# Kernel optimization log

Measured on AMD Instinct MI355X. Metric: run time of the kernel, lower is better.

The kernel has to match this reference:

```python
import jax, jax.numpy as jnp
import numpy as np
import math

B, S, HID = 1, 2048, 1024
H = 16
D = HID // H          # head_dim = 64
M = 128               # RFF num_features
SIGMA = 1.0
ALPHA = 0.9
NORMALIZE = True


def setup_inputs() -> dict:
    key = jax.random.key(0)
    ks = jax.random.split(key, 12)
    s = 1.0 / math.sqrt(HID)  # nn.Linear default-ish init scale
    inp = {
        "hidden_states": jax.random.normal(ks[0], (B, S, HID), dtype=jnp.float32),
        "attention_mask": jnp.zeros((B, 1, 1, S), dtype=jnp.float32),  # 0 = attend
        "Wq": jax.random.uniform(ks[1], (HID, HID), minval=-s, maxval=s, dtype=jnp.float32),
        "bq": jnp.zeros((HID,), dtype=jnp.float32),
        "Wk": jax.random.uniform(ks[2], (HID, HID), minval=-s, maxval=s, dtype=jnp.float32),
        "bk": jnp.zeros((HID,), dtype=jnp.float32),
        "Wv": jax.random.uniform(ks[3], (HID, HID), minval=-s, maxval=s, dtype=jnp.float32),
        "bv": jnp.zeros((HID,), dtype=jnp.float32),
        "Wo": jax.random.uniform(ks[4], (HID, HID), minval=-s, maxval=s, dtype=jnp.float32),
        "bo": jnp.zeros((HID,), dtype=jnp.float32),
        # RFF kernel params per head: omega ~ N(0, 1/sigma^2), phase b ~ U[0, 2pi]
        "omega": jax.random.normal(ks[5], (H, D, M), dtype=jnp.float32) / SIGMA,
        "rff_b": jax.random.uniform(ks[6], (H, M), minval=0.0, maxval=2.0 * math.pi, dtype=jnp.float32),
    }
    return inp


def _heads(x):
    # (B, S, HID) -> (B, H, S, D)
    return x.reshape(B, S, H, D).transpose(0, 2, 1, 3)


def _phi(x, omega, rff_b):
    # x: (B, H, S, D) -> (B, H, S, M) random Fourier features
    proj = jnp.einsum("bhsd,hdm->bhsm", x, omega) + rff_b[None, :, None, :]
    phi = math.sqrt(2.0 / M) * jnp.cos(proj)
    if NORMALIZE:
        phi = phi / (jnp.linalg.norm(phi, axis=-1, keepdims=True) + 1e-6)
    return phi


def reference(hidden_states, attention_mask, Wq, bq, Wk, bk, Wv, bv, Wo, bo, omega, rff_b):
    q = _heads(hidden_states @ Wq.T + bq)   # (B,H,S,D)
    k = _heads(hidden_states @ Wk.T + bk)
    v = _heads(hidden_states @ Wv.T + bv)

    qn = q / (jnp.linalg.norm(q, axis=-1, keepdims=True) + 1e-6)
    kn = k / (jnp.linalg.norm(k, axis=-1, keepdims=True) + 1e-6)

    dot_scores = jnp.einsum("bhqd,bhkd->bhqk", q, k)             # standard QK^T
    kernel_scores = jnp.einsum("bhqm,bhkm->bhqk",
                               _phi(qn, omega, rff_b),
                               _phi(kn, omega, rff_b))            # phi(Q)phi(K)^T

    scores = (ALPHA * dot_scores + (1.0 - ALPHA) * kernel_scores) / math.sqrt(D)
    scores = scores + attention_mask * -10000.0
    weights = jax.nn.softmax(scores, axis=-1)                     # dropout: eval mode (identity)

    context = jnp.einsum("bhqk,bhkd->bhqd", weights, v)
    context = context.transpose(0, 2, 1, 3).reshape(B, S, HID)
    return context @ Wo.T + bo
```

## Files before the change

kernel.cpp:

```cpp
#include <hip/hip_runtime.h>
#include <math.h>

#define S_LEN 2048
#define HID   1024
#define NH    16
#define HD    64
#define NM    128
#define CAUG  192
#define NCH   32

constexpr float ALPHA = 0.9f;

typedef __attribute__((ext_vector_type(8))) short bf16x8;
typedef __attribute__((ext_vector_type(4))) short bf16x4;
typedef __attribute__((ext_vector_type(4))) float f32x4;
typedef __attribute__((ext_vector_type(4))) int   int4v;

#define MFMA(a,b,c) __builtin_amdgcn_mfma_f32_16x16x32_bf16(a,b,c,0,0,0)

static __device__ inline short f2bf(float f) {
    unsigned u = __float_as_uint(f);
    u += 0x7fffu + ((u >> 16) & 1u);
    return (short)(u >> 16);
}
static __device__ inline float bf2f(short s) {
    return __uint_as_float(((unsigned)(unsigned short)s) << 16);
}

__global__ __launch_bounds__(256)
void conv_kernel(const float* __restrict__ hs,
                 const float* __restrict__ Wq, const float* __restrict__ Wk,
                 const float* __restrict__ Wv, const float* __restrict__ Wo,
                 const float* __restrict__ omega,
                 short* __restrict__ hsb, short* __restrict__ wqb, short* __restrict__ wkb,
                 short* __restrict__ wvb, short* __restrict__ wob, short* __restrict__ omtb)
{
    int i = blockIdx.x * 256 + threadIdx.x;
    if (i >= 1605632) return;
    if (i >= 1572864) {
        int j = (i - 1572864) * 4;
        int h = j >> 13, rem = j & 8191;
        int d = rem >> 7, m = rem & 127;
        float4 v = *(const float4*)(omega + j);
        short* dst = omtb + ((h * 128 + m) << 6) + d;
        dst[0]       = f2bf(v.x);
        dst[64]      = f2bf(v.y);
        dst[128]     = f2bf(v.z);
        dst[192]     = f2bf(v.w);
        return;
    }
    const float* src; short* dst; int off;
    if (i < 524288) { src = hs; dst = hsb; off = i; }
    else {
        int j = i - 524288;
        int r = j >> 18;
        off = j & 262143;
        src = (r == 0) ? Wq : (r == 1) ? Wk : (r == 2) ? Wv : Wo;
        dst = (r == 0) ? wqb : (r == 1) ? wkb : (r == 2) ? wvb : wob;
    }
    float4 v = ((const float4*)src)[off];
    bf16x4 o; o[0] = f2bf(v.x); o[1] = f2bf(v.y); o[2] = f2bf(v.z); o[3] = f2bf(v.w);
    ((bf16x4*)dst)[off] = o;
}

__global__ __launch_bounds__(256)
void gemm_mfma(const short* __restrict__ A,
               const short* __restrict__ W0, const float* __restrict__ b0, void* C0,
               const short* __restrict__ W1, const float* __restrict__ b1, void* C1,
               const short* __restrict__ W2, const float* __restrict__ b2, void* C2,
               int m0_, int m1_, int m2_, int Mrows)
{
    const short* W; const float* bias; void* C; int mode;
    if (blockIdx.z == 0)      { W = W0; bias = b0; C = C0; mode = m0_; }
    else if (blockIdx.z == 1) { W = W1; bias = b1; C = C1; mode = m1_; }
    else                      { W = W2; bias = b2; C = C2; mode = m2_; }

    __shared__ short As[128][40];
    __shared__ short Bs[128][40];

    const int tid = threadIdx.x;
    const int wave = tid >> 6, lane = tid & 63;
    const int l15 = lane & 15, l4 = lane >> 4;
    const int wm = wave >> 1, wn = wave & 1;
    const int m0 = blockIdx.y * 128, n0 = blockIdx.x * 128;

    const int srow = (tid >> 2);
    const int scol = (tid & 3) * 16;

    f32x4 acc[4][4];
#pragma unroll
    for (int i = 0; i < 4; ++i)
#pragma unroll
        for (int j = 0; j < 4; ++j) acc[i][j] = (f32x4){0.f,0.f,0.f,0.f};

    int4v apre[2], bpre[2];
#pragma unroll
    for (int it = 0; it < 2; ++it) {
        apre[it] = *(const int4v*)((const char*)A + (size_t)(m0 + srow + it*64) * 2048 + scol);
        bpre[it] = *(const int4v*)((const char*)W + (size_t)(n0 + srow + it*64) * 2048 + scol);
    }

    for (int ks = 0; ks < 32; ++ks) {
        __syncthreads();
#pragma unroll
        for (int it = 0; it < 2; ++it) {
            *(int4v*)((char*)&As[0][0] + (srow + it*64) * 80 + scol) = apre[it];
            *(int4v*)((char*)&Bs[0][0] + (srow + it*64) * 80 + scol) = bpre[it];
        }
        __syncthreads();
        if (ks + 1 < 32) {
            const int kb = (ks + 1) * 64;
#pragma unroll
            for (int it = 0; it < 2; ++it) {
                apre[it] = *(const int4v*)((const char*)A + (size_t)(m0 + srow + it*64) * 2048 + kb + scol);
                bpre[it] = *(const int4v*)((const char*)W + (size_t)(n0 + srow + it*64) * 2048 + kb + scol);
            }
        }
        bf16x8 af[4], bf[4];
#pragma unroll
        for (int mi = 0; mi < 4; ++mi)
            af[mi] = *(const bf16x8*)((const char*)&As[0][0] + (wm*64 + mi*16 + l15) * 80 + l4*16);
#pragma unroll
        for (int nj = 0; nj < 4; ++nj)
            bf[nj] = *(const bf16x8*)((const char*)&Bs[0][0] + (wn*64 + nj*16 + l15) * 80 + l4*16);
#pragma unroll
        for (int mi = 0; mi < 4; ++mi)
#pragma unroll
            for (int nj = 0; nj < 4; ++nj)
                acc[mi][nj] = MFMA(af[mi], bf[nj], acc[mi][nj]);
    }

#pragma unroll
    for (int nj = 0; nj < 4; ++nj) {
        const int nglob = n0 + wn*64 + nj*16 + l15;
        const float bn = bias[nglob];
#pragma unroll
        for (int mi = 0; mi < 4; ++mi) {
            const int mbase = m0 + wm*64 + mi*16 + l4*4;
            if (mode == 0) {
#pragma unroll
                for (int r = 0; r < 4; ++r)
                    ((short*)C)[(size_t)(mbase + r) * 1024 + nglob] = f2bf(acc[mi][nj][r] + bn);
            } else if (mode == 1) {
                bf16x4 pk;
#pragma unroll
                for (int r = 0; r < 4; ++r) pk[r] = f2bf(acc[mi][nj][r] + bn);
                *(bf16x4*)((short*)C + (size_t)nglob * Mrows + mbase) = pk;
            } else {
#pragma unroll
                for (int r = 0; r < 4; ++r)
                    ((float*)C)[(size_t)(mbase + r) * 1024 + nglob] = acc[mi][nj][r] + bn;
            }
        }
    }
}

__global__ __launch_bounds__(256)
void phi2_kernel(const short* __restrict__ qbuf, const short* __restrict__ kbuf,
                 const short* __restrict__ omtb, const float* __restrict__ rffb,
                 short* __restrict__ Qa, short* __restrict__ Ka)
{
    __shared__ short om[128][72];
    __shared__ float bsh[128];

    const int src = blockIdx.z, h = blockIdx.y;
    const int s0 = blockIdx.x * 64;
    const short* X = src ? kbuf : qbuf;
    short* Out     = src ? Ka : Qa;
    const float fq   = src ? 1.0f : (ALPHA * 0.125f);
    const float fphi = src ? 1.0f : ((1.0f - ALPHA) * 0.125f);

    const int tid = threadIdx.x, wave = tid >> 6, lane = tid & 63;
    const int l15 = lane & 15, l4 = lane >> 4;

    {
        const char* gsrc = (const char*)(omtb + ((size_t)h << 13));
#pragma unroll
        for (int it = 0; it < 4; ++it) {
            int f = tid * 16 + it * 4096;
            int row = f >> 7, colb = f & 127;
            *(int4v*)((char*)&om[0][0] + row * 144 + colb) = *(const int4v*)(gsrc + f);
        }
        if (tid < 128) bsh[tid] = rffb[h * 128 + tid];
    }
    __syncthreads();

    const int srow = s0 + wave * 16 + l15;

    bf16x8 xf[2];
#pragma unroll
    for (int cs = 0; cs < 2; ++cs)
        xf[cs] = *(const bf16x8*)(X + (size_t)srow * HID + h * HD + cs * 32 + l4 * 8);

    float ss = 0.f;
#pragma unroll
    for (int cs = 0; cs < 2; ++cs)
#pragma unroll
        for (int j = 0; j < 8; ++j) { float v = bf2f(xf[cs][j]); ss = fmaf(v, v, ss); }
    ss += __shfl_xor(ss, 16);
    ss += __shfl_xor(ss, 32);
    const float inv = 1.0f / (sqrtf(ss) + 1e-6f);

    bf16x8 qn[2];
#pragma unroll
    for (int cs = 0; cs < 2; ++cs) {
        bf16x8 o, w;
#pragma unroll
        for (int j = 0; j < 8; ++j) {
            float v = bf2f(xf[cs][j]);
            o[j] = f2bf(v * inv);
            w[j] = f2bf(v * fq);
        }
        qn[cs] = o;
        *(bf16x8*)(Out + ((size_t)h * S_LEN + srow) * CAUG + cs * 32 + l4 * 8) = w;
    }

    f32x4 pacc[8];
#pragma unroll
    for (int t = 0; t < 8; ++t) pacc[t] = (f32x4){0.f,0.f,0.f,0.f};
#pragma unroll
    for (int t = 0; t < 8; ++t)
#pragma unroll
        for (int cs = 0; cs < 2; ++cs) {
            bf16x8 bf = *(const bf16x8*)((const char*)&om[0][0] + (t*16 + l15) * 144 + cs*64 + l4*16);
            pacc[t] = MFMA(qn[cs], bf, pacc[t]);
        }

    float ph[8][4];
    float ps[4] = {0.f, 0.f, 0.f, 0.f};
#pragma unroll
    for (int t = 0; t < 8; ++t) {
        const float bv = bsh[t * 16 + l15];
#pragma unroll
        for (int r = 0; r < 4; ++r) {
            float p = pacc[t][r] + bv;
            float c = 0.125f * __cosf(p);
            ph[t][r] = c;
            ps[r] = fmaf(c, c, ps[r]);
        }
    }
#pragma unroll
    for (int r = 0; r < 4; ++r) {
        ps[r] += __shfl_xor(ps[r], 1);
        ps[r] += __shfl_xor(ps[r], 2);
        ps[r] += __shfl_xor(ps[r], 4);
        ps[r] += __shfl_xor(ps[r], 8);
    }
    float inv2[4];
#pragma unroll
    for (int r = 0; r < 4; ++r) inv2[r] = fphi / (sqrtf(ps[r]) + 1e-6f);

#pragma unroll
    for (int t = 0; t < 8; ++t)
#pragma unroll
        for (int r = 0; r < 4; ++r)
            Out[((size_t)h * S_LEN + s0 + wave * 16 + l4 * 4 + r) * CAUG + 64 + t * 16 + l15]
                = f2bf(ph[t][r] * inv2[r]);
}

__global__ __launch_bounds__(256, 2)
void flash_mfma(const short* __restrict__ Qa, const short* __restrict__ Ka,
                const short* __restrict__ vt, const float* __restrict__ mask,
                short* __restrict__ ctxb)
{
    __shared__ char smem[61440];

    const int tid = threadIdx.x;
    const int wave = tid >> 6, lane = tid & 63;
    const int l15 = lane & 15, l4 = lane >> 4;
    const int g = wave >> 1, sub = wave & 1;
    const int h = blockIdx.y;
    const int q0 = blockIdx.x * 64 + sub * 32;

    char* PlW  = smem + wave * 2560;
    char* bufA = smem + 10240 + g * 25600;
    char* bufB = bufA + 12800;

    bf16x8 qf[2][6];
#pragma unroll
    for (int qj = 0; qj < 2; ++qj)
#pragma unroll
        for (int cs = 0; cs < 6; ++cs)
            qf[qj][cs] = *(const bf16x8*)(Qa + ((size_t)h * 2048 + q0 + qj*16 + l15) * CAUG + cs*32 + l4*8);

    f32x4 oacc[4][2];
#pragma unroll
    for (int di = 0; di < 4; ++di)
#pragma unroll
        for (int qj = 0; qj < 2; ++qj) oacc[di][qj] = (f32x4){0.f,0.f,0.f,0.f};
    float lsum[2] = {0.f, 0.f};

    const int t = tid & 127;
    int kr[6], kcb[6];
#pragma unroll
    for (int it = 0; it < 6; ++it) { int f = t*16 + it*2048; kr[it] = f/384; kcb[it] = f%384; }

    const char* Kg = (const char*)(Ka + (size_t)h * 2048 * CAUG);
    const char* Vg = (const char*)(vt + (size_t)h * 64 * 2048);
    const int base = g * NCH;

    int4v kpre[6];
    bf16x8 vA[4], vB[4];

    auto loadKpre = [&](int kt) {
        const char* kb = Kg + (size_t)kt * 12288;
#pragma unroll
        for (int it = 0; it < 6; ++it)
            kpre[it] = *(const int4v*)(kb + (size_t)kr[it]*384 + kcb[it]);
    };
    auto writeStage = [&](char* buf) {
#pragma unroll
        for (int it = 0; it < 6; ++it)
            *(int4v*)(buf + kr[it]*400 + kcb[it]) = kpre[it];
    };
    auto loadV = [&](bf16x8 (&dst)[4], int kt) {
#pragma unroll
        for (int di = 0; di < 4; ++di)
            dst[di] = *(const bf16x8*)(Vg + (size_t)(di*16 + l15)*4096 + kt*64 + l4*16);
    };
    auto computeChunk = [&](const char* buf, const bf16x8 (&vf)[4], int kt) {
        f32x4 sacc[2][2];
#pragma unroll
        for (int fi = 0; fi < 2; ++fi)
#pragma unroll
            for (int qj = 0; qj < 2; ++qj) sacc[fi][qj] = (f32x4){0.f,0.f,0.f,0.f};
#pragma unroll
        for (int cs = 0; cs < 6; ++cs) {
            bf16x8 ka[2];
#pragma unroll
            for (int fi = 0; fi < 2; ++fi)
                ka[fi] = *(const bf16x8*)(buf + (fi*16 + l15)*400 + cs*64 + l4*16);
#pragma unroll
            for (int fi = 0; fi < 2; ++fi)
#pragma unroll
                for (int qj = 0; qj < 2; ++qj)
                    sacc[fi][qj] = MFMA(ka[fi], qf[qj][cs], sacc[fi][qj]);
        }
#pragma unroll
        for (int fi = 0; fi < 2; ++fi) {
            float4 mk = *(const float4*)&mask[kt*32 + fi*16 + l4*4];
            float mv[4] = {mk.x * -10000.f, mk.y * -10000.f, mk.z * -10000.f, mk.w * -10000.f};
#pragma unroll
            for (int qj = 0; qj < 2; ++qj) {
                bf16x4 pk;
#pragma unroll
                for (int r = 0; r < 4; ++r) {
                    float p = __expf(sacc[fi][qj][r] + mv[r]);
                    lsum[qj] += p;
                    pk[r] = f2bf(p);
                }
                *(bf16x4*)(PlW + (qj*16 + l15)*80 + fi*32 + l4*8) = pk;
            }
        }
        bf16x8 pb[2];
#pragma unroll
        for (int qj = 0; qj < 2; ++qj)
            pb[qj] = *(const bf16x8*)(PlW + (qj*16 + l15)*80 + l4*16);
#pragma unroll
        for (int di = 0; di < 4; ++di)
#pragma unroll
            for (int qj = 0; qj < 2; ++qj)
                oacc[di][qj] = MFMA(vf[di], pb[qj], oacc[di][qj]);
    };

    loadKpre(base);
    writeStage(bufA);
    loadV(vA, base);
    __syncthreads();

    for (int i = 0; i < NCH; i += 2) {
        loadKpre(base + i + 1);
        loadV(vB, base + i + 1);
        computeChunk(bufA, vA, base + i);
        writeStage(bufB);
        __syncthreads();
        if (i + 2 < NCH) {
            loadKpre(base + i + 2);
            loadV(vA, base + i + 2);
        }
        computeChunk(bufB, vB, base + i + 1);
        if (i + 2 < NCH) writeStage(bufA);
        __syncthreads();
    }

#pragma unroll
    for (int qj = 0; qj < 2; ++qj) {
        lsum[qj] += __shfl_xor(lsum[qj], 16);
        lsum[qj] += __shfl_xor(lsum[qj], 32);
    }

    float* scrO = (float*)(smem + 10240);
    float* scrL = (float*)(smem + 36352);
    if (g == 1) {
#pragma unroll
        for (int qj = 0; qj < 2; ++qj) {
#pragma unroll
            for (int di = 0; di < 4; ++di)
                *(f32x4*)&scrO[(size_t)(sub*32 + qj*16 + l15)*68 + di*16 + l4*4] = oacc[di][qj];
            if (l4 == 0) scrL[sub*32 + qj*16 + l15] = lsum[qj];
        }
    }
    __syncthreads();
    if (g == 0) {
#pragma unroll
        for (int qj = 0; qj < 2; ++qj) {
            const float l = lsum[qj] + scrL[sub*32 + qj*16 + l15];
            const float inv = 1.0f / l;
            const int s = q0 + qj*16 + l15;
#pragma unroll
            for (int di = 0; di < 4; ++di) {
                f32x4 o2 = *(const f32x4*)&scrO[(size_t)(sub*32 + qj*16 + l15)*68 + di*16 + l4*4];
                bf16x4 ob;
#pragma unroll
                for (int r = 0; r < 4; ++r) ob[r] = f2bf((oacc[di][qj][r] + o2[r]) * inv);
                *(bf16x4*)(ctxb + (size_t)s * HID + h*64 + di*16 + l4*4) = ob;
            }
        }
    }
}

extern "C" void kernel_launch(void* const* d_in, const int* in_sizes, int n_in,
                              void* d_out, int out_size, void* d_ws, size_t ws_size,
                              hipStream_t stream)
{
    const float* hs    = (const float*)d_in[0];
    const float* mask  = (const float*)d_in[1];
    const float* Wq    = (const float*)d_in[2];
    const float* bq    = (const float*)d_in[3];
    const float* Wk    = (const float*)d_in[4];
    const float* bk    = (const float*)d_in[5];
    const float* Wv    = (const float*)d_in[6];
    const float* bv    = (const float*)d_in[7];
    const float* Wo    = (const float*)d_in[8];
    const float* bo    = (const float*)d_in[9];
    const float* omega = (const float*)d_in[10];
    const float* rffb  = (const float*)d_in[11];
    float* out = (float*)d_out;

    short* wsS = (short*)d_ws;
    short* hsb = wsS;
    short* wqb = hsb + 2097152;
    short* wkb = wqb + 1048576;
    short* wvb = wkb + 1048576;
    short* wob = wvb + 1048576;
    short* qb  = wob + 1048576;
    short* kb  = qb  + 2097152;
    short* vtb = kb  + 2097152;
    short* ctxb= vtb + 2097152;
    short* QaB = ctxb+ 2097152;
    short* KaB = QaB + 6291456;
    short* omtb= KaB + 6291456;

    conv_kernel<<<6272, 256, 0, stream>>>(hs, Wq, Wk, Wv, Wo, omega,
                                          hsb, wqb, wkb, wvb, wob, omtb);
    gemm_mfma<<<dim3(8, 16, 3), 256, 0, stream>>>(hsb, wqb, bq, qb, wkb, bk, kb, wvb, bv, vtb,
                                                  0, 0, 1, S_LEN);
    phi2_kernel<<<dim3(32, 16, 2), 256, 0, stream>>>(qb, kb, omtb, rffb, QaB, KaB);
    flash_mfma<<<dim3(32, 16), 256, 0, stream>>>(QaB, KaB, vtb, mask, ctxb);
    gemm_mfma<<<dim3(8, 16, 1), 256, 0, stream>>>(ctxb, wob, bo, out, wob, bo, out, wob, bo, out,
                                                  2, 2, 2, S_LEN);
}
```

Measured before the change: 135.8 us.

## Fuse fp32-to-bf16 conversion into GEMM loads and split flash attention over keys

The standalone conversion kernel is removed. GEMMs now read fp32 inputs and weights directly and convert them to bf16 while loading, and the GEMM tile shrinks to 64x128 so each launch has twice as many blocks. Flash attention is split into two key halves along grid z, with smaller shared memory so that four blocks can run per CU. Each half writes bf16 partial outputs and row sums, and a new merge kernel combines them. The aim is to skip the extra conversion pass and raise occupancy, at the cost of the double-buffered K/V prefetch, one extra kernel launch, and rounding the partial outputs to bf16 before the merge.

```diff
diff --git a/kernel.cpp b/kernel.cpp
--- a/kernel.cpp
+++ b/kernel.cpp
@@ -7,7 +7,7 @@
 #define HD    64
 #define NM    128
 #define CAUG  192
-#define NCH   32
+#define NCHW  16
 
 constexpr float ALPHA = 0.9f;
 
@@ -28,103 +28,85 @@
 }
 
 __global__ __launch_bounds__(256)
-void conv_kernel(const float* __restrict__ hs,
-                 const float* __restrict__ Wq, const float* __restrict__ Wk,
-                 const float* __restrict__ Wv, const float* __restrict__ Wo,
-                 const float* __restrict__ omega,
-                 short* __restrict__ hsb, short* __restrict__ wqb, short* __restrict__ wkb,
-                 short* __restrict__ wvb, short* __restrict__ wob, short* __restrict__ omtb)
+void omt_kernel(const float* __restrict__ omega, short* __restrict__ omtb)
 {
     int i = blockIdx.x * 256 + threadIdx.x;
-    if (i >= 1605632) return;
-    if (i >= 1572864) {
-        int j = (i - 1572864) * 4;
-        int h = j >> 13, rem = j & 8191;
-        int d = rem >> 7, m = rem & 127;
-        float4 v = *(const float4*)(omega + j);
-        short* dst = omtb + ((h * 128 + m) << 6) + d;
-        dst[0]       = f2bf(v.x);
-        dst[64]      = f2bf(v.y);
-        dst[128]     = f2bf(v.z);
-        dst[192]     = f2bf(v.w);
-        return;
-    }
-    const float* src; short* dst; int off;
-    if (i < 524288) { src = hs; dst = hsb; off = i; }
-    else {
-        int j = i - 524288;
-        int r = j >> 18;
-        off = j & 262143;
-        src = (r == 0) ? Wq : (r == 1) ? Wk : (r == 2) ? Wv : Wo;
-        dst = (r == 0) ? wqb : (r == 1) ? wkb : (r == 2) ? wvb : wob;
-    }
-    float4 v = ((const float4*)src)[off];
-    bf16x4 o; o[0] = f2bf(v.x); o[1] = f2bf(v.y); o[2] = f2bf(v.z); o[3] = f2bf(v.w);
-    ((bf16x4*)dst)[off] = o;
+    if (i >= 131072) return;
+    int h = i >> 13, rem = i & 8191;
+    int d = rem >> 7, m = rem & 127;
+    omtb[((h * 128 + m) << 6) + d] = f2bf(omega[i]);
 }
 
 __global__ __launch_bounds__(256)
-void gemm_mfma(const short* __restrict__ A,
-               const short* __restrict__ W0, const float* __restrict__ b0, void* C0,
-               const short* __restrict__ W1, const float* __restrict__ b1, void* C1,
-               const short* __restrict__ W2, const float* __restrict__ b2, void* C2,
+void gemm_mfma(const void* __restrict__ Ax, int a_f32,
+               const float* __restrict__ W0, const float* __restrict__ b0, void* C0,
+               const float* __restrict__ W1, const float* __restrict__ b1, void* C1,
+               const float* __restrict__ W2, const float* __restrict__ b2, void* C2,
                int m0_, int m1_, int m2_, int Mrows)
 {
-    const short* W; const float* bias; void* C; int mode;
+    const float* W; const float* bias; void* C; int mode;
     if (blockIdx.z == 0)      { W = W0; bias = b0; C = C0; mode = m0_; }
     else if (blockIdx.z == 1) { W = W1; bias = b1; C = C1; mode = m1_; }
     else                      { W = W2; bias = b2; C = C2; mode = m2_; }
 
-    __shared__ short As[128][40];
+    __shared__ short As[64][40];
     __shared__ short Bs[128][40];
 
     const int tid = threadIdx.x;
     const int wave = tid >> 6, lane = tid & 63;
     const int l15 = lane & 15, l4 = lane >> 4;
     const int wm = wave >> 1, wn = wave & 1;
-    const int m0 = blockIdx.y * 128, n0 = blockIdx.x * 128;
-
-    const int srow = (tid >> 2);
-    const int scol = (tid & 3) * 16;
-
-    f32x4 acc[4][4];
-#pragma unroll
-    for (int i = 0; i < 4; ++i)
+    const int m0 = blockIdx.y * 64, n0 = blockIdx.x * 128;
+
+    const int srow = tid >> 2;
+    const int se   = (tid & 3) * 8;
+
+    f32x4 acc[2][4];
+#pragma unroll
+    for (int i = 0; i < 2; ++i)
 #pragma unroll
         for (int j = 0; j < 4; ++j) acc[i][j] = (f32x4){0.f,0.f,0.f,0.f};
 
-    int4v apre[2], bpre[2];
-#pragma unroll
-    for (int it = 0; it < 2; ++it) {
-        apre[it] = *(const int4v*)((const char*)A + (size_t)(m0 + srow + it*64) * 2048 + scol);
-        bpre[it] = *(const int4v*)((const char*)W + (size_t)(n0 + srow + it*64) * 2048 + scol);
-    }
+    auto cvt8 = [](float4 f0, float4 f1) -> int4v {
+        bf16x8 c;
+        c[0]=f2bf(f0.x); c[1]=f2bf(f0.y); c[2]=f2bf(f0.z); c[3]=f2bf(f0.w);
+        c[4]=f2bf(f1.x); c[5]=f2bf(f1.y); c[6]=f2bf(f1.z); c[7]=f2bf(f1.w);
+        return *(int4v*)&c;
+    };
+    auto ldA = [&](int ks) -> int4v {
+        if (a_f32) {
+            const float* p = (const float*)Ax + (size_t)(m0 + srow) * 1024 + ks * 32 + se;
+            return cvt8(*(const float4*)p, *(const float4*)(p + 4));
+        }
+        return *(const int4v*)((const char*)Ax + (size_t)(m0 + srow) * 2048 + ks * 64 + se * 2);
+    };
+    auto ldW = [&](int ks, int rofs) -> int4v {
+        const float* p = W + (size_t)(n0 + rofs + srow) * 1024 + ks * 32 + se;
+        return cvt8(*(const float4*)p, *(const float4*)(p + 4));
+    };
+
+    int4v apre = ldA(0), bpre0 = ldW(0, 0), bpre1 = ldW(0, 64);
 
     for (int ks = 0; ks < 32; ++ks) {
         __syncthreads();
-#pragma unroll
-        for (int it = 0; it < 2; ++it) {
-            *(int4v*)((char*)&As[0][0] + (srow + it*64) * 80 + scol) = apre[it];
-            *(int4v*)((char*)&Bs[0][0] + (srow + it*64) * 80 + scol) = bpre[it];
-        }
+        *(int4v*)((char*)&As[0][0] + srow * 80 + se * 2) = apre;
+        *(int4v*)((char*)&Bs[0][0] + srow * 80 + se * 2) = bpre0;
+        *(int4v*)((char*)&Bs[0][0] + (64 + srow) * 80 + se * 2) = bpre1;
         __syncthreads();
         if (ks + 1 < 32) {
-            const int kb = (ks + 1) * 64;
-#pragma unroll
-            for (int it = 0; it < 2; ++it) {
-                apre[it] = *(const int4v*)((const char*)A + (size_t)(m0 + srow + it*64) * 2048 + kb + scol);
-                bpre[it] = *(const int4v*)((const char*)W + (size_t)(n0 + srow + it*64) * 2048 + kb + scol);
-            }
-        }
-        bf16x8 af[4], bf[4];
-#pragma unroll
-        for (int mi = 0; mi < 4; ++mi)
-            af[mi] = *(const bf16x8*)((const char*)&As[0][0] + (wm*64 + mi*16 + l15) * 80 + l4*16);
+            apre  = ldA(ks + 1);
+            bpre0 = ldW(ks + 1, 0);
+            bpre1 = ldW(ks + 1, 64);
+        }
+        bf16x8 af[2], bf[4];
+#pragma unroll
+        for (int mi = 0; mi < 2; ++mi)
+            af[mi] = *(const bf16x8*)((const char*)&As[0][0] + (wm*32 + mi*16 + l15) * 80 + l4*16);
 #pragma unroll
         for (int nj = 0; nj < 4; ++nj)
             bf[nj] = *(const bf16x8*)((const char*)&Bs[0][0] + (wn*64 + nj*16 + l15) * 80 + l4*16);
 #pragma unroll
-        for (int mi = 0; mi < 4; ++mi)
+        for (int mi = 0; mi < 2; ++mi)
 #pragma unroll
             for (int nj = 0; nj < 4; ++nj)
                 acc[mi][nj] = MFMA(af[mi], bf[nj], acc[mi][nj]);
@@ -135,8 +117,8 @@
         const int nglob = n0 + wn*64 + nj*16 + l15;
         const float bn = bias[nglob];
 #pragma unroll
-        for (int mi = 0; mi < 4; ++mi) {
-            const int mbase = m0 + wm*64 + mi*16 + l4*4;
+        for (int mi = 0; mi < 2; ++mi) {
+            const int mbase = m0 + wm*32 + mi*16 + l4*4;
             if (mode == 0) {
 #pragma unroll
                 for (int r = 0; r < 4; ++r)
@@ -258,23 +240,23 @@
                 = f2bf(ph[t][r] * inv2[r]);
 }
 
-__global__ __launch_bounds__(256, 2)
+__global__ __launch_bounds__(256, 4)
 void flash_mfma(const short* __restrict__ Qa, const short* __restrict__ Ka,
                 const short* __restrict__ vt, const float* __restrict__ mask,
-                short* __restrict__ ctxb)
-{
-    __shared__ char smem[61440];
+                short* __restrict__ Opart, float* __restrict__ Lpart)
+{
+    __shared__ char smem[35840];
 
     const int tid = threadIdx.x;
     const int wave = tid >> 6, lane = tid & 63;
     const int l15 = lane & 15, l4 = lane >> 4;
     const int g = wave >> 1, sub = wave & 1;
     const int h = blockIdx.y;
+    const int ksp = blockIdx.z;
     const int q0 = blockIdx.x * 64 + sub * 32;
 
-    char* PlW  = smem + wave * 2560;
-    char* bufA = smem + 10240 + g * 25600;
-    char* bufB = bufA + 12800;
+    char* Kbuf = smem + g * 12800;
+    char* PlW  = smem + 25600 + wave * 2560;
 
     bf16x8 qf[2][6];
 #pragma unroll
@@ -297,28 +279,27 @@
 
     const char* Kg = (const char*)(Ka + (size_t)h * 2048 * CAUG);
     const char* Vg = (const char*)(vt + (size_t)h * 64 * 2048);
-    const int base = g * NCH;
+    const int base = ksp * 32 + g * NCHW;
 
     int4v kpre[6];
-    bf16x8 vA[4], vB[4];
-
     auto loadKpre = [&](int kt) {
         const char* kb = Kg + (size_t)kt * 12288;
 #pragma unroll
         for (int it = 0; it < 6; ++it)
             kpre[it] = *(const int4v*)(kb + (size_t)kr[it]*384 + kcb[it]);
     };
-    auto writeStage = [&](char* buf) {
+
+    loadKpre(base);
+
+    for (int i = 0; i < NCHW; ++i) {
+        const int kt = base + i;
+        __syncthreads();
 #pragma unroll
         for (int it = 0; it < 6; ++it)
-            *(int4v*)(buf + kr[it]*400 + kcb[it]) = kpre[it];
-    };
-    auto loadV = [&](bf16x8 (&dst)[4], int kt) {
-#pragma unroll
-        for (int di = 0; di < 4; ++di)
-            dst[di] = *(const bf16x8*)(Vg + (size_t)(di*16 + l15)*4096 + kt*64 + l4*16);
-    };
-    auto computeChunk = [&](const char* buf, const bf16x8 (&vf)[4], int kt) {
+            *(int4v*)(Kbuf + kr[it]*400 + kcb[it]) = kpre[it];
+        __syncthreads();
+        if (i + 1 < NCHW) loadKpre(kt + 1);
+
         f32x4 sacc[2][2];
 #pragma unroll
         for (int fi = 0; fi < 2; ++fi)
@@ -329,7 +310,7 @@
             bf16x8 ka[2];
 #pragma unroll
             for (int fi = 0; fi < 2; ++fi)
-                ka[fi] = *(const bf16x8*)(buf + (fi*16 + l15)*400 + cs*64 + l4*16);
+                ka[fi] = *(const bf16x8*)(Kbuf + (fi*16 + l15)*400 + cs*64 + l4*16);
 #pragma unroll
             for (int fi = 0; fi < 2; ++fi)
 #pragma unroll
@@ -352,35 +333,19 @@
                 *(bf16x4*)(PlW + (qj*16 + l15)*80 + fi*32 + l4*8) = pk;
             }
         }
-        bf16x8 pb[2];
-#pragma unroll
-        for (int qj = 0; qj < 2; ++qj)
-            pb[qj] = *(const bf16x8*)(PlW + (qj*16 + l15)*80 + l4*16);
-#pragma unroll
-        for (int di = 0; di < 4; ++di)
+        {
+            bf16x8 pb[2];
 #pragma unroll
             for (int qj = 0; qj < 2; ++qj)
-                oacc[di][qj] = MFMA(vf[di], pb[qj], oacc[di][qj]);
-    };
-
-    loadKpre(base);
-    writeStage(bufA);
-    loadV(vA, base);
-    __syncthreads();
-
-    for (int i = 0; i < NCH; i += 2) {
-        loadKpre(base + i + 1);
-        loadV(vB, base + i + 1);
-        computeChunk(bufA, vA, base + i);
-        writeStage(bufB);
-        __syncthreads();
-        if (i + 2 < NCH) {
-            loadKpre(base + i + 2);
-            loadV(vA, base + i + 2);
-        }
-        computeChunk(bufB, vB, base + i + 1);
-        if (i + 2 < NCH) writeStage(bufA);
-        __syncthreads();
+                pb[qj] = *(const bf16x8*)(PlW + (qj*16 + l15)*80 + l4*16);
+#pragma unroll
+            for (int di = 0; di < 4; ++di) {
+                bf16x8 va = *(const bf16x8*)(Vg + (size_t)(di*16 + l15)*4096 + kt*64 + l4*16);
+#pragma unroll
+                for (int qj = 0; qj < 2; ++qj)
+                    oacc[di][qj] = MFMA(va, pb[qj], oacc[di][qj]);
+            }
+        }
     }
 
 #pragma unroll
@@ -389,34 +354,68 @@
         lsum[qj] += __shfl_xor(lsum[qj], 32);
     }
 
-    float* scrO = (float*)(smem + 10240);
-    float* scrL = (float*)(smem + 36352);
+    __syncthreads();
+    float* scrO = (float*)smem;
+    float* scrL = (float*)(smem + 25600);
     if (g == 1) {
 #pragma unroll
         for (int qj = 0; qj < 2; ++qj) {
+            const int row = sub*32 + qj*16 + l15;
 #pragma unroll
             for (int di = 0; di < 4; ++di)
-                *(f32x4*)&scrO[(size_t)(sub*32 + qj*16 + l15)*68 + di*16 + l4*4] = oacc[di][qj];
-            if (l4 == 0) scrL[sub*32 + qj*16 + l15] = lsum[qj];
+                *(f32x4*)&scrO[(size_t)row*68 + di*16 + l4*4] = oacc[di][qj];
+            if (l4 == 0) scrL[row] = lsum[qj];
         }
     }
     __syncthreads();
     if (g == 0) {
 #pragma unroll
         for (int qj = 0; qj < 2; ++qj) {
-            const float l = lsum[qj] + scrL[sub*32 + qj*16 + l15];
-            const float inv = 1.0f / l;
-            const int s = q0 + qj*16 + l15;
+            const int row = sub*32 + qj*16 + l15;
+            const float l = lsum[qj] + scrL[row];
 #pragma unroll
             for (int di = 0; di < 4; ++di) {
-                f32x4 o2 = *(const f32x4*)&scrO[(size_t)(sub*32 + qj*16 + l15)*68 + di*16 + l4*4];
-                bf16x4 ob;
-#pragma unroll
-                for (int r = 0; r < 4; ++r) ob[r] = f2bf((oacc[di][qj][r] + o2[r]) * inv);
-                *(bf16x4*)(ctxb + (size_t)s * HID + h*64 + di*16 + l4*4) = ob;
+                f32x4 o2 = *(const f32x4*)&scrO[(size_t)row*68 + di*16 + l4*4];
+                *(f32x4*)&scrO[(size_t)row*68 + di*16 + l4*4] = oacc[di][qj] + o2;
             }
-        }
-    }
+            if (l4 == 0) scrL[row] = l;
+        }
+    }
+    __syncthreads();
+    if (tid < 128) {
+        const size_t obase = ((size_t)(ksp * NH + h) * 2048 + blockIdx.x * 64);
+#pragma unroll
+        for (int it2 = 0; it2 < 8; ++it2) {
+            int idx = it2 * 128 + tid;
+            int q = idx >> 4, dc = (idx & 15) * 4;
+            f32x4 v = *(const f32x4*)&scrO[(size_t)q*68 + dc];
+            bf16x4 ob;
+#pragma unroll
+            for (int r = 0; r < 4; ++r) ob[r] = f2bf(v[r]);
+            *(bf16x4*)(Opart + (obase + q) * 64 + dc) = ob;
+        }
+        if (tid < 64) Lpart[obase + tid] = scrL[tid];
+    }
+}
+
+__global__ __launch_bounds__(256)
+void merge_kernel(const short* __restrict__ Opart, const float* __restrict__ Lpart,
+                  short* __restrict__ ctxb)
+{
+    int tt = blockIdx.x * 256 + threadIdx.x;
+    int e = tt * 4;
+    int d = e & 63;
+    int q = (e >> 6) & 2047;
+    int h = e >> 17;
+    size_t i0 = (size_t)h * 2048 + q;
+    size_t i1 = (size_t)(NH + h) * 2048 + q;
+    bf16x4 a = *(const bf16x4*)(Opart + i0 * 64 + d);
+    bf16x4 b = *(const bf16x4*)(Opart + i1 * 64 + d);
+    float inv = 1.0f / (Lpart[i0] + Lpart[i1]);
+    bf16x4 o;
+#pragma unroll
+    for (int r = 0; r < 4; ++r) o[r] = f2bf((bf2f(a[r]) + bf2f(b[r])) * inv);
+    *(bf16x4*)(ctxb + (size_t)q * 1024 + h * 64 + d) = o;
 }
 
 extern "C" void kernel_launch(void* const* d_in, const int* in_sizes, int n_in,
@@ -437,26 +436,23 @@
     const float* rffb  = (const float*)d_in[11];
     float* out = (float*)d_out;
 
-    short* wsS = (short*)d_ws;
-    short* hsb = wsS;
-    short* wqb = hsb + 2097152;
-    short* wkb = wqb + 1048576;
-    short* wvb = wkb + 1048576;
-    short* wob = wvb + 1048576;
-    short* qb  = wob + 1048576;
-    short* kb  = qb  + 2097152;
-    short* vtb = kb  + 2097152;
-    short* ctxb= vtb + 2097152;
-    short* QaB = ctxb+ 2097152;
-    short* KaB = QaB + 6291456;
-    short* omtb= KaB + 6291456;
-
-    conv_kernel<<<6272, 256, 0, stream>>>(hs, Wq, Wk, Wv, Wo, omega,
-                                          hsb, wqb, wkb, wvb, wob, omtb);
-    gemm_mfma<<<dim3(8, 16, 3), 256, 0, stream>>>(hsb, wqb, bq, qb, wkb, bk, kb, wvb, bv, vtb,
+    short* wsS  = (short*)d_ws;
+    short* qb   = wsS;
+    short* kb   = qb   + 2097152;
+    short* vtb  = kb   + 2097152;
+    short* ctxb = vtb  + 2097152;
+    short* QaB  = ctxb + 2097152;
+    short* KaB  = QaB  + 6291456;
+    short* omtb = KaB  + 6291456;
+    short* OpS  = omtb + 131072;
+    float* LpF  = (float*)(OpS + 4194304);
+
+    omt_kernel<<<512, 256, 0, stream>>>(omega, omtb);
+    gemm_mfma<<<dim3(8, 32, 3), 256, 0, stream>>>(hs, 1, Wq, bq, qb, Wk, bk, kb, Wv, bv, vtb,
                                                   0, 0, 1, S_LEN);
     phi2_kernel<<<dim3(32, 16, 2), 256, 0, stream>>>(qb, kb, omtb, rffb, QaB, KaB);
-    flash_mfma<<<dim3(32, 16), 256, 0, stream>>>(QaB, KaB, vtb, mask, ctxb);
-    gemm_mfma<<<dim3(8, 16, 1), 256, 0, stream>>>(ctxb, wob, bo, out, wob, bo, out, wob, bo, out,
+    flash_mfma<<<dim3(32, 16, 2), 256, 0, stream>>>(QaB, KaB, vtb, mask, OpS, LpF);
+    merge_kernel<<<2048, 256, 0, stream>>>(OpS, LpF, ctxb);
+    gemm_mfma<<<dim3(8, 32, 1), 256, 0, stream>>>(ctxb, 0, Wo, bo, out, Wo, bo, out, Wo, bo, out,
                                                   2, 2, 2, S_LEN);
 }
```

New measurement: 198.8 us. +46.4%, slower.
